# Optimization experiments

Hardware: AMD Instinct MI355X
Metric: run time of the kernel (lower is better)

Reference implementation:

```python
import jax, jax.numpy as jnp
import numpy as np

HEADS = 8
VTH = 1.0
TAU = 2.0          # spikingjelly LIFNode default tau
RS = 64            # region size for bi-level routing
TOPK = 4           # routed regions per query region
ALPHA = 2.0        # ATan surrogate alpha


@jax.custom_vjp
def spike(x):
    # Heaviside forward, ATan surrogate backward (spikingjelly surrogate.ATan)
    return (x >= 0.0).astype(x.dtype)

def _spike_fwd(x):
    return spike(x), x

def _spike_bwd(x, g):
    return (g * (ALPHA / 2.0) / (1.0 + (jnp.pi / 2.0 * ALPHA * x) ** 2),)

spike.defvjp(_spike_fwd, _spike_bwd)


def lif(x):
    # x: [Lt, b, L, dim]; multi-step LIF, v_reset=0 hard reset, detach_reset=True
    def step(v, xt):
        v = v + (xt - v) / TAU
        s = spike(v - VTH)
        v = v * (1.0 - jax.lax.stop_gradient(s))
        return v, s
    _, s = jax.lax.scan(step, jnp.zeros_like(x[0]), x)
    return s


def batchnorm(x, gamma, beta, eps=1e-5):
    # BatchNorm1d(dim) applied to [Lt*b, dim, L]: stats over (Lt, b, L) per channel
    mean = x.mean(axis=(0, 1, 2), keepdims=True)
    var = x.var(axis=(0, 1, 2), keepdims=True)
    return (x - mean) * jax.lax.rsqrt(var + eps) * gamma + beta


def bilevel_attn(s, Wqkv, bqkv, Wo, bo):
    Lt, b, L, dim = s.shape
    R = L // RS
    hd = dim // HEADS
    q, k, v = jnp.split(s @ Wqkv + bqkv, 3, axis=-1)            # each [Lt,b,L,dim]
    # coarse region-level routing on mean-pooled q/k
    qr = q.reshape(Lt, b, R, RS, dim).mean(3)                    # [Lt,b,R,dim]
    kr = k.reshape(Lt, b, R, RS, dim).mean(3)
    aff = jnp.einsum('tbrd,tbsd->tbrs', qr, kr)                  # [Lt,b,R,R]
    _, idx = jax.lax.top_k(aff, TOPK)                            # [Lt,b,R,TOPK]
    kreg = k.reshape(Lt, b, R, RS, HEADS, hd)
    vreg = v.reshape(Lt, b, R, RS, HEADS, hd)
    gidx = idx[:, :, :, :, None, None, None]
    kg = jnp.take_along_axis(kreg[:, :, None], gidx, axis=3).reshape(Lt, b, R, TOPK * RS, HEADS, hd)
    vg = jnp.take_along_axis(vreg[:, :, None], gidx, axis=3).reshape(Lt, b, R, TOPK * RS, HEADS, hd)
    qt = q.reshape(Lt, b, R, RS, HEADS, hd)
    scores = jnp.einsum('tbrihd,tbrjhd->tbrhij', qt, kg) / np.sqrt(hd).astype(np.float32)
    p = jax.nn.softmax(scores, axis=-1)
    out = jnp.einsum('tbrhij,tbrjhd->tbrihd', p, vg).reshape(Lt, b, L, dim)
    return out @ Wo + bo


def _block(x, bn1_gamma, bn1_beta, Wqkv, bqkv, Wo, bo,
           bn2_gamma, bn2_beta, W1, b1, W2, b2, scale):
    s1 = lif(batchnorm(x, bn1_gamma, bn1_beta))
    x = x + bilevel_attn(s1, Wqkv, bqkv, Wo, bo) * scale
    s2 = lif(batchnorm(x, bn2_gamma, bn2_beta))
    h = jax.nn.gelu(s2 @ W1 + b1, approximate=False)
    x = x + (h @ W2 + b2) * scale
    return x


def setup_inputs() -> dict:
    key = jax.random.key(0)
    ks = jax.random.split(key, 8)
    Lt, b, L, dim = 4, 8, 1024, 256
    x = jax.random.normal(ks[0], (Lt, b, L, dim), dtype=jnp.float32)
    w = lambda k, sh: 0.02 * jax.random.normal(k, sh, dtype=jnp.float32)
    return {
        'x': x,
        'bn1_gamma': jnp.ones((dim,), jnp.float32),
        'bn1_beta': jnp.zeros((dim,), jnp.float32),
        'Wqkv': w(ks[1], (dim, 3 * dim)),
        'bqkv': jnp.zeros((3 * dim,), jnp.float32),
        'Wo': w(ks[2], (dim, dim)),
        'bo': jnp.zeros((dim,), jnp.float32),
        'bn2_gamma': jnp.ones((dim,), jnp.float32),
        'bn2_beta': jnp.zeros((dim,), jnp.float32),
        'W1': w(ks[3], (dim, 4 * dim)),
        'b1': jnp.zeros((4 * dim,), jnp.float32),
        'W2': w(ks[4], (4 * dim, dim)),
        'b2': jnp.zeros((dim,), jnp.float32),
        'scale': jnp.array(0.5, jnp.float32),
        'Lt': Lt, 'b': b, 'L': L, 'dim': dim,
    }


def reference(x, bn1_gamma, bn1_beta, Wqkv, bqkv, Wo, bo,
              bn2_gamma, bn2_beta, W1, b1, W2, b2, scale,
              Lt, b, L, dim):
    return _block(x, bn1_gamma, bn1_beta, Wqkv, bqkv, Wo, bo,
                  bn2_gamma, bn2_beta, W1, b1, W2, b2, scale)
```

## Files before the change

kernel.cpp:

```cpp
#include <hip/hip_runtime.h>
#include <hip/hip_bf16.h>
#include <math.h>

typedef __hip_bfloat16 bf16;
typedef unsigned long long u64;
typedef unsigned int u32;

#define LTT 4
#define DIM 256
#define NTOK 32768
#define MT 2097152
#define NTOT 8388608

typedef __attribute__((ext_vector_type(8))) short short8;
typedef __attribute__((ext_vector_type(4))) float f32x4;
typedef __attribute__((ext_vector_type(4))) u32 u32x4;

__device__ __forceinline__ float ldin(const void* p, size_t i, int f) {
  float v = f ? ((const float*)p)[i] : __bfloat162float(((const bf16*)p)[i]);
  return isfinite(v) ? v : 0.0f;
}

__device__ __forceinline__ short bf16bits(float x) {
  union { bf16 b; short s; } u; u.b = __float2bfloat16(x); return u.s;
}

struct PtrPack { const void* p[14]; int n[14]; };

__global__ void probe_all_k(PtrPack pk, int* flags) {
  int b = blockIdx.x;
  int tid = threadIdx.x;
  const unsigned short* u = (const unsigned short*)pk.p[b];
  int nelem = pk.n[b];
  int n = nelem < 1024 ? nelem : 1024;
  bool big = false, nz = false;
  for (int i = tid; i < n; i += 64) {
    unsigned short h = u[i];
    if (((h >> 7) & 0xFF) >= 0xC0) big = true;
    if (h != 0) nz = true;
  }
  u64 bm = __ballot(big);
  u64 zm = __ballot(nz);
  if (tid == 0) {
    unsigned short h0 = u[0];
    int f = 0;
    if (bm != 0ull) f = 1;
    else if (h0 == 0 && (zm != 0ull || n == 1)) f = 1;
    flags[b] = f;
    if (b == 0) flags[15] = 1;
  }
}

__global__ void __launch_bounds__(1024)
bnstats_k(const void* __restrict__ x, const int* __restrict__ fxp,
          float* __restrict__ gsum, float* __restrict__ gsq) {
  int fx = *fxp;
  int c = threadIdx.x & 255;
  int part = threadIdx.x >> 8;
  int tok0 = blockIdx.x * 128 + part * 32;
  float s = 0.f, q = 0.f;
  for (int t = 0; t < 32; t++) {
    float v = ldin(x, (size_t)(tok0 + t) * DIM + c, fx);
    s += v; q += v * v;
  }
  __shared__ float ls[4][256], lq[4][256];
  ls[part][c] = s; lq[part][c] = q;
  __syncthreads();
  if (threadIdx.x < 256) {
    float S = ls[0][c] + ls[1][c] + ls[2][c] + ls[3][c];
    float Q = lq[0][c] + lq[1][c] + lq[2][c] + lq[3][c];
    atomicAdd(&gsum[c], S);
    atomicAdd(&gsq[c], Q);
  }
}

__global__ void lif_k(const void* __restrict__ x, const int* __restrict__ fxp,
                      const float* __restrict__ gsum, const float* __restrict__ gsq,
                      const void* __restrict__ gamma, const int* __restrict__ fgp,
                      const void* __restrict__ beta, const int* __restrict__ fbp,
                      u64* __restrict__ bits) {
  int fx = *fxp, fg = *fgp, fb = *fbp;
  int m = blockIdx.x * 256 + threadIdx.x;
  int c = m & (DIM - 1);
  int lane = threadIdx.x & 63;
  float mean = gsum[c] * (1.0f / 32768.0f);
  float var  = gsq[c] * (1.0f / 32768.0f) - mean * mean;
  float inv  = rsqrtf(var + 1e-5f);
  float g = ldin(gamma, c, fg), be = ldin(beta, c, fb);
  float v = 0.f;
  #pragma unroll
  for (int t = 0; t < LTT; t++) {
    size_t e = (size_t)t * MT + m;
    float xn = (ldin(x, e, fx) - mean) * inv * g + be;
    v = v + (xn - v) * 0.5f;
    bool sp = (v - 1.0f >= 0.0f);
    u64 bl = __ballot(sp);
    if (lane == 0) bits[e >> 6] = bl;
    v = sp ? 0.0f : v;
  }
}

__device__ __forceinline__ float gelu_f(float x) {
  return 0.5f * x * (1.0f + erff(x * 0.70710678118654752440f));
}

__global__ void wconv_all_k(const void* __restrict__ Wqkv, const void* __restrict__ Wo,
                            const void* __restrict__ W1, const void* __restrict__ W2,
                            const int* __restrict__ flags,
                            bf16* __restrict__ wqkvt, bf16* __restrict__ wot,
                            bf16* __restrict__ w1t, bf16* __restrict__ w2t) {
  int b = blockIdx.x, t = threadIdx.x;
  const void* W; const int* f; bf16* o; int K, N, n, kblk = 0;
  if (b < 768)       { W = Wqkv; f = flags + 3;  o = wqkvt; K = 256;  N = 768;  n = b; }
  else if (b < 1024) { W = Wo;   f = flags + 5;  o = wot;   K = 256;  N = 256;  n = b - 768; }
  else if (b < 2048) { W = W1;   f = flags + 9;  o = w1t;   K = 256;  N = 1024; n = b - 1024; }
  else { W = W2; f = flags + 11; o = w2t; K = 1024; N = 256;
         int q = b - 2048; kblk = q >> 8; n = q & 255; }
  int k = kblk * 256 + t;
  o[(size_t)n * K + k] = __float2bfloat16(ldin(W, (size_t)k * N + n, *f));
}

template <int MODE, int ABITS>
__global__ void __launch_bounds__(256)
dgemm_k(const void* __restrict__ Av, const bf16* __restrict__ Bt,
        const void* __restrict__ biasv, const int* __restrict__ fbp,
        void* O, const void* xinv, const int* __restrict__ fxp,
        const void* __restrict__ scalev, const int* __restrict__ fsp,
        int N, int K, size_t obase) {
  int tid = threadIdx.x;
  int lane = tid & 63, w = tid >> 6;
  int wr = w >> 1, wc = w & 1;
  int kq = lane >> 4, lr = lane & 15;
  int bm = blockIdx.y * 128, bn = blockIdx.x * 128;
  f32x4 acc[4][4] = {};

  if constexpr (ABITS) {
    __shared__ __align__(16) short lut[256][8];
    {
      short8 e;
      #pragma unroll
      for (int j = 0; j < 8; j++) e[j] = ((tid >> j) & 1) ? (short)0x3F80 : (short)0;
      *(short8*)&lut[tid][0] = e;
    }
    const u32* Abits = (const u32*)Av;
    u32 ab[4][8];
    #pragma unroll
    for (int i = 0; i < 4; i++) {
      const u32* rp = &Abits[(size_t)(bm + wr * 64 + i * 16 + lr) * 8];
      *(u32x4*)&ab[i][0] = *(const u32x4*)&rp[0];
      *(u32x4*)&ab[i][4] = *(const u32x4*)&rp[4];
    }
    __syncthreads();
    #pragma unroll
    for (int s = 0; s < 8; s++) {
      short8 af[4], bf[4];
      #pragma unroll
      for (int i = 0; i < 4; i++) {
        u32 byte = (ab[i][s] >> (kq * 8)) & 0xFFu;
        af[i] = *(const short8*)&lut[byte][0];
      }
      #pragma unroll
      for (int j = 0; j < 4; j++)
        bf[j] = *(const short8*)&Bt[(size_t)(bn + wc * 64 + j * 16 + lr) * 256 + s * 32 + kq * 8];
      #pragma unroll
      for (int i = 0; i < 4; i++)
        #pragma unroll
        for (int j = 0; j < 4; j++)
          acc[i][j] = __builtin_amdgcn_mfma_f32_16x16x32_bf16(af[i], bf[j], acc[i][j], 0, 0, 0);
    }
  } else {
    const bf16* Ab = (const bf16*)Av;
    for (int k0 = 0; k0 < K; k0 += 32) {
      short8 af[4], bf[4];
      #pragma unroll
      for (int i = 0; i < 4; i++)
        af[i] = *(const short8*)&Ab[(size_t)(bm + wr * 64 + i * 16 + lr) * K + k0 + kq * 8];
      #pragma unroll
      for (int j = 0; j < 4; j++)
        bf[j] = *(const short8*)&Bt[(size_t)(bn + wc * 64 + j * 16 + lr) * K + k0 + kq * 8];
      #pragma unroll
      for (int i = 0; i < 4; i++)
        #pragma unroll
        for (int j = 0; j < 4; j++)
          acc[i][j] = __builtin_amdgcn_mfma_f32_16x16x32_bf16(af[i], bf[j], acc[i][j], 0, 0, 0);
    }
  }

  float scl = 0.f;
  int fx = 0, fbias = *fbp;
  if (MODE == 4) { scl = ldin(scalev, 0, *fsp); fx = *fxp; }
  int row0 = bm + wr * 64 + kq * 4;
  int col0 = bn + wc * 64 + lr;
  #pragma unroll
  for (int j = 0; j < 4; j++) {
    int n = col0 + j * 16;
    float bb = ldin(biasv, n, fbias);
    #pragma unroll
    for (int i = 0; i < 4; i++) {
      #pragma unroll
      for (int r = 0; r < 4; r++) {
        int m = row0 + i * 16 + r;
        float v = acc[i][j][r] + bb;
        size_t o = obase + (size_t)m * N + n;
        if (MODE == 2) {
          ((bf16*)O)[o] = __float2bfloat16(gelu_f(v));
        } else if (MODE == 3) {
          ((bf16*)O)[o] = __float2bfloat16(v);
        } else {
          float base = ldin(xinv, o, fx);
          ((float*)O)[o] = base + scl * v;
        }
      }
    }
  }
}

__global__ void __launch_bounds__(512)
ffn_k(const u64* __restrict__ bits_, const bf16* __restrict__ w1t,
      const void* __restrict__ b1v, const int* __restrict__ f1p,
      const bf16* __restrict__ w2t,
      const void* __restrict__ b2v, const int* __restrict__ f2p,
      float* out, const void* __restrict__ scalev, const int* __restrict__ fsp) {
  __shared__ __align__(16) short lut[256][8];
  __shared__ __align__(16) short As[32][64][8];
  __shared__ __align__(16) short hl[2][16][64][8];
  int tid = threadIdx.x;
  int lane = tid & 63, w = tid >> 6;
  int kq = lane >> 4, lr = lane & 15;
  int m0 = blockIdx.x * 64;
  if (tid < 256) {
    short8 e;
    #pragma unroll
    for (int j = 0; j < 8; j++) e[j] = ((tid >> j) & 1) ? (short)0x3F80 : (short)0;
    *(short8*)&lut[tid][0] = e;
  }
  __syncthreads();
  {
    int row = tid >> 3, word = tid & 7;
    u32 val = ((const u32*)bits_)[(size_t)(m0 + row) * 8 + word];
    #pragma unroll
    for (int q = 0; q < 4; q++) {
      u32 byte = (val >> (q * 8)) & 0xFFu;
      *(short8*)&As[word * 4 + q][row][0] = *(const short8*)&lut[byte][0];
    }
  }
  int f1 = *f1p;
  f32x4 acc2[4][2] = {};
  __syncthreads();

  for (int c = 0; c < 8; c++) {
    f32x4 accA[4] = {};
    #pragma unroll
    for (int s = 0; s < 8; s++) {
      short8 bfw = *(const short8*)&w1t[(size_t)(c * 128 + w * 16 + lr) * 256 + s * 32 + kq * 8];
      #pragma unroll
      for (int i = 0; i < 4; i++) {
        short8 af = *(const short8*)&As[s * 4 + kq][i * 16 + lr][0];
        accA[i] = __builtin_amdgcn_mfma_f32_16x16x32_bf16(af, bfw, accA[i], 0, 0, 0);
      }
    }
    {
      int cl = w * 16 + lr;
      float bb = ldin(b1v, c * 128 + cl, f1);
      #pragma unroll
      for (int i = 0; i < 4; i++)
        #pragma unroll
        for (int r = 0; r < 4; r++)
          hl[c & 1][cl >> 3][i * 16 + kq * 4 + r][cl & 7] = bf16bits(gelu_f(accA[i][r] + bb));
    }
    short8 pb[4][2];
    #pragma unroll
    for (int ks = 0; ks < 4; ks++) {
      pb[ks][0] = *(const short8*)&w2t[(size_t)(w * 32 + lr) * 1024 + c * 128 + ks * 32 + kq * 8];
      pb[ks][1] = *(const short8*)&w2t[(size_t)(w * 32 + 16 + lr) * 1024 + c * 128 + ks * 32 + kq * 8];
    }
    __syncthreads();
    #pragma unroll
    for (int ks = 0; ks < 4; ks++) {
      #pragma unroll
      for (int i = 0; i < 4; i++) {
        short8 af = *(const short8*)&hl[c & 1][ks * 4 + kq][i * 16 + lr][0];
        acc2[i][0] = __builtin_amdgcn_mfma_f32_16x16x32_bf16(af, pb[ks][0], acc2[i][0], 0, 0, 0);
        acc2[i][1] = __builtin_amdgcn_mfma_f32_16x16x32_bf16(af, pb[ks][1], acc2[i][1], 0, 0, 0);
      }
    }
  }

  float scl = ldin(scalev, 0, *fsp);
  int f2 = *f2p;
  #pragma unroll
  for (int j = 0; j < 2; j++) {
    int n = w * 32 + j * 16 + lr;
    float bb = ldin(b2v, n, f2);
    #pragma unroll
    for (int i = 0; i < 4; i++)
      #pragma unroll
      for (int r = 0; r < 4; r++) {
        int row = m0 + i * 16 + kq * 4 + r;
        size_t o = (size_t)row * 256 + n;
        out[o] = out[o] + scl * (acc2[i][j][r] + bb);
      }
  }
}

__global__ void regmean_k(const u64* __restrict__ bits, float* __restrict__ sreg) {
  int blk = blockIdx.x;
  int c = threadIdx.x;
  float s = 0.f;
  for (int i = 0; i < 64; i++) {
    u64 w = bits[(size_t)(blk * 64 + i) * 4 + (c >> 6)];
    s += (float)((w >> (c & 63)) & 1ull);
  }
  sreg[(size_t)blk * 256 + c] = s * (1.0f / 64.0f);
}

__global__ void __launch_bounds__(256)
pgemm_k(const float* __restrict__ A,
        const void* __restrict__ Bv, const int* __restrict__ fBp,
        const void* __restrict__ biasv, const int* __restrict__ fbp,
        float* __restrict__ Oq) {
  int fB = *fBp, fb = *fbp;
  __shared__ float Ast[16][68];
  __shared__ float Bs[16][68];
  int tid = threadIdx.x;
  int bm = blockIdx.y * 64, bn = blockIdx.x * 64;
  int tr = tid >> 4, tc = tid & 15;
  float acc[4][4] = {};
  for (int k0 = 0; k0 < 256; k0 += 16) {
    for (int t = tid; t < 1024; t += 256) {
      int m = t >> 4, k = t & 15;
      Ast[k][m] = A[(size_t)(bm + m) * 256 + k0 + k];
    }
    for (int t = tid; t < 1024; t += 256) {
      int k = t >> 6, n = t & 63;
      Bs[k][n] = ldin(Bv, (size_t)(k0 + k) * 768 + bn + n, fB);
    }
    __syncthreads();
    #pragma unroll
    for (int kk = 0; kk < 16; kk++) {
      float4 a4 = *(const float4*)&Ast[kk][tr * 4];
      float4 b4 = *(const float4*)&Bs[kk][tc * 4];
      float a[4] = {a4.x, a4.y, a4.z, a4.w};
      float b[4] = {b4.x, b4.y, b4.z, b4.w};
      #pragma unroll
      for (int i = 0; i < 4; i++)
        #pragma unroll
        for (int jj = 0; jj < 4; jj++)
          acc[i][jj] += a[i] * b[jj];
    }
    __syncthreads();
  }
  #pragma unroll
  for (int i = 0; i < 4; i++)
    #pragma unroll
    for (int jj = 0; jj < 4; jj++) {
      int n = bn + tc * 4 + jj;
      Oq[(size_t)(bm + tr * 4 + i) * 512 + n] = acc[i][jj] + ldin(biasv, n, fb);
    }
}

__global__ void afftopk_k(const float* __restrict__ qkr, int* __restrict__ idx) {
  int blk = blockIdx.x;
  int tb = blk >> 4;
  int tid = threadIdx.x;
  int s_ = tid >> 4, p = tid & 15;
  __shared__ float part[256];
  __shared__ float aff[16];
  const float* qrow = qkr + (size_t)blk * 512;
  const float* krow = qkr + (size_t)(tb * 16 + s_) * 512 + 256;
  float acc = 0.f;
  for (int c = p * 16; c < p * 16 + 16; c++) acc += qrow[c] * krow[c];
  part[tid] = acc;
  __syncthreads();
  if (tid < 16) {
    float a = 0.f;
    for (int pp = 0; pp < 16; pp++) a += part[tid * 16 + pp];
    aff[tid] = a;
  }
  __syncthreads();
  if (tid == 0) {
    bool taken[16] = {};
    for (int kk = 0; kk < 4; kk++) {
      float best = -INFINITY; int bi = 0;
      for (int i = 0; i < 16; i++)
        if (!taken[i] && aff[i] > best) { best = aff[i]; bi = i; }
      taken[bi] = true;
      idx[blk * 4 + kk] = bi;
    }
  }
}

__global__ void __launch_bounds__(256)
attn_k(const bf16* __restrict__ qkv, const int* __restrict__ idx,
       bf16* __restrict__ ctx) {
  __shared__ __align__(16) short Ks[256][32];
  __shared__ __align__(16) short Vs[32][256];
  __shared__ __align__(16) short Ps[4][16][256];
  int blk = blockIdx.x;
  int h = blk & 7, br = blk >> 3;
  int b = br >> 4;
  int tid = threadIdx.x;
  int base = br * 64;
  int r0 = idx[br * 4 + 0], r1 = idx[br * 4 + 1];
  int r2 = idx[br * 4 + 2], r3 = idx[br * 4 + 3];

  #pragma unroll
  for (int c = 0; c < 4; c++) {
    int g = c * 256 + tid;
    int tk = g >> 2, ch = g & 3;
    int rs = tk >> 6;
    int rid = (rs & 2) ? ((rs & 1) ? r3 : r2) : ((rs & 1) ? r1 : r0);
    int gt = b * 1024 + rid * 64 + (tk & 63);
    short8 v = *(const short8*)&qkv[(size_t)gt * 768 + 256 + h * 32 + ch * 8];
    *(short8*)&Ks[tk][ch * 8] = v;
  }
  {
    int tk = tid;
    int rs = tk >> 6;
    int rid = (rs & 2) ? ((rs & 1) ? r3 : r2) : ((rs & 1) ? r1 : r0);
    int gt = b * 1024 + rid * 64 + (tk & 63);
    const bf16* vp = &qkv[(size_t)gt * 768 + 512 + h * 32];
    short vv[32];
    *(short8*)&vv[0]  = *(const short8*)&vp[0];
    *(short8*)&vv[8]  = *(const short8*)&vp[8];
    *(short8*)&vv[16] = *(const short8*)&vp[16];
    *(short8*)&vv[24] = *(const short8*)&vp[24];
    #pragma unroll
    for (int d = 0; d < 32; d++)
      Vs[d][(tk + 8 * d) & 255] = vv[d];
  }
  __syncthreads();

  int w = tid >> 6, lane = tid & 63, kq = lane >> 4, lr = lane & 15;

  short8 qf = *(const short8*)&qkv[(size_t)(base + w * 16 + lr) * 768 + h * 32 + kq * 8];

  f32x4 s[16];
  #pragma unroll
  for (int nt = 0; nt < 16; nt++) {
    short8 kf = *(const short8*)&Ks[nt * 16 + lr][kq * 8];
    f32x4 z = {0.f, 0.f, 0.f, 0.f};
    s[nt] = __builtin_amdgcn_mfma_f32_16x16x32_bf16(qf, kf, z, 0, 0, 0);
  }

  const float cs = 0.17677669529663687f;
  float mx[4] = {-INFINITY, -INFINITY, -INFINITY, -INFINITY};
  #pragma unroll
  for (int nt = 0; nt < 16; nt++)
    #pragma unroll
    for (int r = 0; r < 4; r++) mx[r] = fmaxf(mx[r], s[nt][r]);
  #pragma unroll
  for (int m = 1; m < 16; m <<= 1)
    #pragma unroll
    for (int r = 0; r < 4; r++) mx[r] = fmaxf(mx[r], __shfl_xor(mx[r], m, 64));
  float sum[4] = {0.f, 0.f, 0.f, 0.f};
  #pragma unroll
  for (int nt = 0; nt < 16; nt++)
    #pragma unroll
    for (int r = 0; r < 4; r++) {
      float e = __expf((s[nt][r] - mx[r]) * cs);
      s[nt][r] = e; sum[r] += e;
    }
  #pragma unroll
  for (int m = 1; m < 16; m <<= 1)
    #pragma unroll
    for (int r = 0; r < 4; r++) sum[r] += __shfl_xor(sum[r], m, 64);
  float inv[4];
  #pragma unroll
  for (int r = 0; r < 4; r++) inv[r] = 1.0f / sum[r];

  #pragma unroll
  for (int nt = 0; nt < 16; nt++)
    #pragma unroll
    for (int r = 0; r < 4; r++) {
      int row = kq * 4 + r;
      int col = nt * 16 + lr;
      Ps[w][row][col ^ ((row & 7) << 3)] = bf16bits(s[nt][r] * inv[r]);
    }
  __syncthreads();

  f32x4 o0 = {0.f, 0.f, 0.f, 0.f}, o1 = {0.f, 0.f, 0.f, 0.f};
  #pragma unroll
  for (int kc = 0; kc < 8; kc++) {
    short8 pf = *(const short8*)
        &Ps[w][lr][(kc ^ ((lr >> 2) & 1)) * 32 + (kq ^ (lr & 3)) * 8];
    int d0 = lr, d1 = 16 + lr;
    short8 vf0 = *(const short8*)&Vs[d0][(kc * 32 + kq * 8 + 8 * d0) & 255];
    short8 vf1 = *(const short8*)&Vs[d1][(kc * 32 + kq * 8 + 8 * d1) & 255];
    o0 = __builtin_amdgcn_mfma_f32_16x16x32_bf16(pf, vf0, o0, 0, 0, 0);
    o1 = __builtin_amdgcn_mfma_f32_16x16x32_bf16(pf, vf1, o1, 0, 0, 0);
  }

  #pragma unroll
  for (int r = 0; r < 4; r++) {
    int q = base + w * 16 + kq * 4 + r;
    ctx[(size_t)q * 256 + h * 32 + lr]      = __float2bfloat16(o0[r]);
    ctx[(size_t)q * 256 + h * 32 + 16 + lr] = __float2bfloat16(o1[r]);
  }
}

extern "C" void kernel_launch(void* const* d_in, const int* in_sizes, int n_in,
                              void* d_out, int out_size, void* d_ws, size_t ws_size,
                              hipStream_t stream) {
  const void* x_in = d_in[0];
  const void* Wqkv = d_in[3];
  const void* bqkv = d_in[4];
  const void* Wo   = d_in[5];
  const void* bo   = d_in[6];
  const void* W1   = d_in[9];
  const void* b1   = d_in[10];
  const void* W2   = d_in[11];
  const void* b2   = d_in[12];
  const void* scale = d_in[13];

  const size_t MISC = 256 + 1048576 + 524288 + 8192 + 1048576 + 2048
                    + 393216 + 131072 + 524288 + 524288;
  int C;
  if      (MISC + (size_t)32 * 2097152 <= ws_size) C = 32;
  else if (MISC + (size_t)16 * 2097152 <= ws_size) C = 16;
  else if (MISC + (size_t)8  * 2097152 <= ws_size) C = 8;
  else if (MISC + (size_t)4  * 2097152 <= ws_size) C = 4;
  else                                             C = 1;
  size_t r0 = (size_t)C * 2097152;

  char* ws = (char*)d_ws;
  int*  flags = (int*)ws;
  char* p = ws + 256;
  bf16* qkvb = (bf16*)p;
  bf16* ctxb = (bf16*)(p + (size_t)C * 1572864);
  p += r0;
  float* qkr  = (float*)p;  p += 1048576;
  float* sreg = (float*)p;  p += 524288;
  int*   idxb = (int*)p;    p += 8192;
  u64*   bits = (u64*)p;    p += 1048576;
  float* gsum = (float*)p;  p += 2048;
  float* gsq  = gsum + 256;
  bf16* wqkvt = (bf16*)p;   p += 393216;
  bf16* wot   = (bf16*)p;   p += 131072;
  bf16* w1t   = (bf16*)p;   p += 524288;
  bf16* w2t   = (bf16*)p;   p += 524288;
  float* out  = (float*)d_out;
  const int* F14 = flags + 14;

  hipMemsetAsync(flags, 0, 256, stream);
  PtrPack pk;
  for (int i = 0; i < 14; i++) { pk.p[i] = d_in[i]; pk.n[i] = in_sizes[i]; }
  probe_all_k<<<14, 64, 0, stream>>>(pk, flags);

  wconv_all_k<<<3072, 256, 0, stream>>>(Wqkv, Wo, W1, W2, flags,
                                        wqkvt, wot, w1t, w2t);

  hipMemsetAsync(gsum, 0, 512 * sizeof(float), stream);
  bnstats_k<<<256, 1024, 0, stream>>>(x_in, flags + 0, gsum, gsq);
  lif_k<<<MT / 256, 256, 0, stream>>>(x_in, flags + 0, gsum, gsq,
                                      d_in[1], flags + 1, d_in[2], flags + 2, bits);

  regmean_k<<<512, 256, 0, stream>>>(bits, sreg);
  pgemm_k<<<dim3(8, 8), 256, 0, stream>>>(sreg, Wqkv, flags + 3, bqkv, flags + 4, qkr);
  afftopk_k<<<512, 256, 0, stream>>>(qkr, idxb);

  for (int gb = 0; gb < 32; gb += C) {
    size_t tok0 = (size_t)gb * 1024;
    dgemm_k<3, 1><<<dim3(6, C * 8), 256, 0, stream>>>(
        (const void*)((const u32*)bits + tok0 * 8), wqkvt,
        bqkv, flags + 4, qkvb, nullptr, F14, nullptr, F14, 768, 256, 0);
    attn_k<<<C * 128, 256, 0, stream>>>(qkvb, idxb + gb * 64, ctxb);
    dgemm_k<4, 0><<<dim3(2, C * 8), 256, 0, stream>>>(
        ctxb, wot, bo, flags + 6, out, x_in, flags + 0,
        scale, flags + 13, 256, 256, tok0 * 256);
  }

  hipMemsetAsync(gsum, 0, 512 * sizeof(float), stream);
  bnstats_k<<<256, 1024, 0, stream>>>(out, flags + 15, gsum, gsq);
  lif_k<<<MT / 256, 256, 0, stream>>>(out, flags + 15, gsum, gsq,
                                      d_in[7], flags + 7, d_in[8], flags + 8, bits);

  ffn_k<<<NTOK / 64, 512, 0, stream>>>(bits, w1t, b1, flags + 10,
                                       w2t, b2, flags + 12,
                                       out, scale, flags + 13);
}
```

Baseline: 416.7 us.

## Fuse second BatchNorm statistics into output-projection GEMM epilogue

The attention output GEMM epilogue now accumulates per-channel sum and sum-of-squares into shared memory and then into global buffers, so the separate second bnstats pass over the 32 MB residual output is removed. LIF now loads all four timesteps up front before the recurrence, to get more loads in flight. The FFN kernel drops the double-buffered hidden tile for a single buffer plus an extra barrier per chunk. The fused stats add shared and global atomics to the GEMM epilogue. Computing the stats from fp32 sums also changes reduction order slightly.

New measurement: 404.1 us. 1.03x faster.

```diff
diff --git a/kernel.cpp b/kernel.cpp
--- a/kernel.cpp
+++ b/kernel.cpp
@@ -87,15 +87,17 @@
   float var  = gsq[c] * (1.0f / 32768.0f) - mean * mean;
   float inv  = rsqrtf(var + 1e-5f);
   float g = ldin(gamma, c, fg), be = ldin(beta, c, fb);
+  float xn[LTT];
+  #pragma unroll
+  for (int t = 0; t < LTT; t++)
+    xn[t] = (ldin(x, (size_t)t * MT + m, fx) - mean) * inv * g + be;
   float v = 0.f;
   #pragma unroll
   for (int t = 0; t < LTT; t++) {
-    size_t e = (size_t)t * MT + m;
-    float xn = (ldin(x, e, fx) - mean) * inv * g + be;
-    v = v + (xn - v) * 0.5f;
+    v = v + (xn[t] - v) * 0.5f;
     bool sp = (v - 1.0f >= 0.0f);
     u64 bl = __ballot(sp);
-    if (lane == 0) bits[e >> 6] = bl;
+    if (lane == 0) bits[((size_t)t * MT + m) >> 6] = bl;
     v = sp ? 0.0f : v;
   }
 }
@@ -126,13 +128,19 @@
         const void* __restrict__ biasv, const int* __restrict__ fbp,
         void* O, const void* xinv, const int* __restrict__ fxp,
         const void* __restrict__ scalev, const int* __restrict__ fsp,
-        int N, int K, size_t obase) {
+        int N, int K, size_t obase,
+        float* __restrict__ gs2, float* __restrict__ gq2) {
   int tid = threadIdx.x;
   int lane = tid & 63, w = tid >> 6;
   int wr = w >> 1, wc = w & 1;
   int kq = lane >> 4, lr = lane & 15;
   int bm = blockIdx.y * 128, bn = blockIdx.x * 128;
   f32x4 acc[4][4] = {};
+  __shared__ float lsum[128], lsq[128];
+  if constexpr (MODE == 5) {
+    if (tid < 128) { lsum[tid] = 0.f; lsq[tid] = 0.f; }
+    __syncthreads();
+  }
 
   if constexpr (ABITS) {
     __shared__ __align__(16) short lut[256][8];
@@ -188,13 +196,14 @@
 
   float scl = 0.f;
   int fx = 0, fbias = *fbp;
-  if (MODE == 4) { scl = ldin(scalev, 0, *fsp); fx = *fxp; }
+  if (MODE >= 4) { scl = ldin(scalev, 0, *fsp); fx = *fxp; }
   int row0 = bm + wr * 64 + kq * 4;
   int col0 = bn + wc * 64 + lr;
   #pragma unroll
   for (int j = 0; j < 4; j++) {
     int n = col0 + j * 16;
     float bb = ldin(biasv, n, fbias);
+    float sj = 0.f, qj = 0.f;
     #pragma unroll
     for (int i = 0; i < 4; i++) {
       #pragma unroll
@@ -202,15 +211,27 @@
         int m = row0 + i * 16 + r;
         float v = acc[i][j][r] + bb;
         size_t o = obase + (size_t)m * N + n;
-        if (MODE == 2) {
-          ((bf16*)O)[o] = __float2bfloat16(gelu_f(v));
-        } else if (MODE == 3) {
+        if (MODE == 3) {
           ((bf16*)O)[o] = __float2bfloat16(v);
         } else {
-          float base = ldin(xinv, o, fx);
-          ((float*)O)[o] = base + scl * v;
+          float basev = ldin(xinv, o, fx);
+          float ov = basev + scl * v;
+          ((float*)O)[o] = ov;
+          sj += ov; qj += ov * ov;
         }
       }
+    }
+    if constexpr (MODE == 5) {
+      int li = wc * 64 + j * 16 + lr;
+      atomicAdd(&lsum[li], sj);
+      atomicAdd(&lsq[li], qj);
+    }
+  }
+  if constexpr (MODE == 5) {
+    __syncthreads();
+    if (tid < 128) {
+      atomicAdd(&gs2[bn + tid], lsum[tid]);
+      atomicAdd(&gq2[bn + tid], lsq[tid]);
     }
   }
 }
@@ -223,7 +244,7 @@
       float* out, const void* __restrict__ scalev, const int* __restrict__ fsp) {
   __shared__ __align__(16) short lut[256][8];
   __shared__ __align__(16) short As[32][64][8];
-  __shared__ __align__(16) short hl[2][16][64][8];
+  __shared__ __align__(16) short hl[16][64][8];
   int tid = threadIdx.x;
   int lane = tid & 63, w = tid >> 6;
   int kq = lane >> 4, lr = lane & 15;
@@ -259,6 +280,7 @@
         accA[i] = __builtin_amdgcn_mfma_f32_16x16x32_bf16(af, bfw, accA[i], 0, 0, 0);
       }
     }
+    __syncthreads();
     {
       int cl = w * 16 + lr;
       float bb = ldin(b1v, c * 128 + cl, f1);
@@ -266,7 +288,7 @@
       for (int i = 0; i < 4; i++)
         #pragma unroll
         for (int r = 0; r < 4; r++)
-          hl[c & 1][cl >> 3][i * 16 + kq * 4 + r][cl & 7] = bf16bits(gelu_f(accA[i][r] + bb));
+          hl[cl >> 3][i * 16 + kq * 4 + r][cl & 7] = bf16bits(gelu_f(accA[i][r] + bb));
     }
     short8 pb[4][2];
     #pragma unroll
@@ -279,7 +301,7 @@
     for (int ks = 0; ks < 4; ks++) {
       #pragma unroll
       for (int i = 0; i < 4; i++) {
-        short8 af = *(const short8*)&hl[c & 1][ks * 4 + kq][i * 16 + lr][0];
+        short8 af = *(const short8*)&hl[ks * 4 + kq][i * 16 + lr][0];
         acc2[i][0] = __builtin_amdgcn_mfma_f32_16x16x32_bf16(af, pb[ks][0], acc2[i][0], 0, 0, 0);
         acc2[i][1] = __builtin_amdgcn_mfma_f32_16x16x32_bf16(af, pb[ks][1], acc2[i][1], 0, 0, 0);
       }
@@ -513,7 +535,7 @@
   const void* b2   = d_in[12];
   const void* scale = d_in[13];
 
-  const size_t MISC = 256 + 1048576 + 524288 + 8192 + 1048576 + 2048
+  const size_t MISC = 256 + 1048576 + 524288 + 8192 + 1048576 + 4096
                     + 393216 + 131072 + 524288 + 524288;
   int C;
   if      (MISC + (size_t)32 * 2097152 <= ws_size) C = 32;
@@ -533,8 +555,10 @@
   float* sreg = (float*)p;  p += 524288;
   int*   idxb = (int*)p;    p += 8192;
   u64*   bits = (u64*)p;    p += 1048576;
-  float* gsum = (float*)p;  p += 2048;
+  float* gsum = (float*)p;  p += 4096;
   float* gsq  = gsum + 256;
+  float* gsum2 = gsum + 512;
+  float* gsq2  = gsum + 768;
   bf16* wqkvt = (bf16*)p;   p += 393216;
   bf16* wot   = (bf16*)p;   p += 131072;
   bf16* w1t   = (bf16*)p;   p += 524288;
@@ -543,6 +567,7 @@
   const int* F14 = flags + 14;
 
   hipMemsetAsync(flags, 0, 256, stream);
+  hipMemsetAsync(gsum, 0, 1024 * sizeof(float), stream);
   PtrPack pk;
   for (int i = 0; i < 14; i++) { pk.p[i] = d_in[i]; pk.n[i] = in_sizes[i]; }
   probe_all_k<<<14, 64, 0, stream>>>(pk, flags);
@@ -550,7 +575,6 @@
   wconv_all_k<<<3072, 256, 0, stream>>>(Wqkv, Wo, W1, W2, flags,
                                         wqkvt, wot, w1t, w2t);
 
-  hipMemsetAsync(gsum, 0, 512 * sizeof(float), stream);
   bnstats_k<<<256, 1024, 0, stream>>>(x_in, flags + 0, gsum, gsq);
   lif_k<<<MT / 256, 256, 0, stream>>>(x_in, flags + 0, gsum, gsq,
                                       d_in[1], flags + 1, d_in[2], flags + 2, bits);
@@ -563,16 +587,15 @@
     size_t tok0 = (size_t)gb * 1024;
     dgemm_k<3, 1><<<dim3(6, C * 8), 256, 0, stream>>>(
         (const void*)((const u32*)bits + tok0 * 8), wqkvt,
-        bqkv, flags + 4, qkvb, nullptr, F14, nullptr, F14, 768, 256, 0);
+        bqkv, flags + 4, qkvb, nullptr, F14, nullptr, F14, 768, 256, 0,
+        nullptr, nullptr);
     attn_k<<<C * 128, 256, 0, stream>>>(qkvb, idxb + gb * 64, ctxb);
-    dgemm_k<4, 0><<<dim3(2, C * 8), 256, 0, stream>>>(
+    dgemm_k<5, 0><<<dim3(2, C * 8), 256, 0, stream>>>(
         ctxb, wot, bo, flags + 6, out, x_in, flags + 0,
-        scale, flags + 13, 256, 256, tok0 * 256);
-  }
-
-  hipMemsetAsync(gsum, 0, 512 * sizeof(float), stream);
-  bnstats_k<<<256, 1024, 0, stream>>>(out, flags + 15, gsum, gsq);
-  lif_k<<<MT / 256, 256, 0, stream>>>(out, flags + 15, gsum, gsq,
+        scale, flags + 13, 256, 256, tok0 * 256, gsum2, gsq2);
+  }
+
+  lif_k<<<MT / 256, 256, 0, stream>>>(out, flags + 15, gsum2, gsq2,
                                       d_in[7], flags + 7, d_in[8], flags + 8, bits);
 
   ffn_k<<<NTOK / 64, 512, 0, stream>>>(bits, w1t, b1, flags + 10,
```
